# Kernel optimization log

Measured on AMD Instinct MI355X. Metric: run time of the kernel, lower is better.

## Reference

```python
import jax, jax.numpy as jnp
import numpy as np

B, S, D = 2, 2048, 2048
H, KV, HD = 8, 1, 256          # num_heads, num_kv_heads, head_dim
ROPE_BASE = 10000.0
NEG_INF = -1e9


def _rope_cos_sin(position_ids, head_dim, base):
    # position_ids: [B, S] -> cos/sin: [B, S, head_dim]
    inv_freq = 1.0 / (base ** (jnp.arange(0, head_dim, 2, dtype=jnp.float32) / head_dim))
    freqs = position_ids.astype(jnp.float32)[..., None] * inv_freq  # [B,S,HD/2]
    emb = jnp.concatenate([freqs, freqs], axis=-1)                  # [B,S,HD]
    return jnp.cos(emb), jnp.sin(emb)


def _rotate_half(x):
    h = x.shape[-1] // 2
    return jnp.concatenate([-x[..., h:], x[..., :h]], axis=-1)


def _apply_rope(x, cos, sin):
    # x: [B,h,S,HD]; cos/sin: [B,S,HD]
    c = cos[:, None, :, :]
    s = sin[:, None, :, :]
    return x * c + _rotate_half(x) * s


def setup_inputs() -> dict:
    key = jax.random.key(0)
    ks = jax.random.split(key, 6)
    hidden_state = jax.random.normal(ks[0], (B, S, D), dtype=jnp.float32)
    # additive causal mask: 0 on/below diagonal, -inf above
    causal = jnp.tril(jnp.ones((S, S), dtype=bool))
    attention_mask = jnp.where(causal, 0.0, NEG_INF).astype(jnp.float32)[None, None]  # [B?1,1,S,S]
    attention_mask = jnp.broadcast_to(attention_mask, (B, 1, S, S))
    position_ids = jnp.broadcast_to(jnp.arange(S, dtype=jnp.int64)[None, :], (B, S))
    scale = 0.02
    Wq = jax.random.normal(ks[1], (D, H * HD), dtype=jnp.float32) * scale
    Wk = jax.random.normal(ks[2], (D, KV * HD), dtype=jnp.float32) * scale
    Wv = jax.random.normal(ks[3], (D, KV * HD), dtype=jnp.float32) * scale
    Wo = jax.random.normal(ks[4], (H * HD, D), dtype=jnp.float32) * scale
    return {"hidden_state": hidden_state, "attention_mask": attention_mask,
            "position_ids": position_ids, "Wq": Wq, "Wk": Wk, "Wv": Wv, "Wo": Wo}


def reference(hidden_state, attention_mask, position_ids, Wq, Wk, Wv, Wo):
    bsz, q_len, _ = hidden_state.shape
    n_rep = H // KV
    # projections
    q = (hidden_state @ Wq).reshape(bsz, q_len, H, HD).transpose(0, 2, 1, 3)   # [B,H,S,HD]
    k = (hidden_state @ Wk).reshape(bsz, q_len, KV, HD).transpose(0, 2, 1, 3)  # [B,KV,S,HD]
    v = (hidden_state @ Wv).reshape(bsz, q_len, KV, HD).transpose(0, 2, 1, 3)
    # RoPE
    cos, sin = _rope_cos_sin(position_ids, HD, ROPE_BASE)
    q = _apply_rope(q, cos, sin)
    k = _apply_rope(k, cos, sin)
    # GQA: repeat kv heads
    k = jnp.repeat(k, n_rep, axis=1)  # [B,H,S,HD]
    v = jnp.repeat(v, n_rep, axis=1)
    # eager attention with full score matrix (faithful to source)
    scores = jnp.einsum('bhqd,bhkd->bhqk', q, k) / jnp.sqrt(jnp.float32(HD))
    scores = scores + attention_mask
    attn = jax.nn.softmax(scores.astype(jnp.float32), axis=-1).astype(q.dtype)
    out = jnp.einsum('bhqk,bhkd->bhqd', attn, v)            # [B,H,S,HD]
    out = out.transpose(0, 2, 1, 3).reshape(bsz, q_len, H * HD)
    return out @ Wo
```

## Files before the change

kernel.cpp:

```cpp
#include <hip/hip_runtime.h>
#include <cstdint>
#include <cstddef>

#define B_   2
#define S_   2048
#define D_   2048
#define H_   8
#define HD_  256
#define M_   (B_ * S_)
#define NQ_  (H_ * HD_)
#define NKV_ 256

typedef unsigned short u16;
typedef __attribute__((ext_vector_type(8))) short short8v;
typedef __attribute__((ext_vector_type(4))) float f32x4;

__device__ __forceinline__ u16 f2bf_rn(float x) {
    unsigned int u = __float_as_uint(x);
    unsigned int r = u + 0x7FFFu + ((u >> 16) & 1u);
    return (u16)(r >> 16);
}
__device__ __forceinline__ float bf2f(u16 h) {
    return __uint_as_float(((unsigned int)h) << 16);
}

__global__ __launch_bounds__(256) void split_kernel(const float* __restrict__ in,
                                                    u16* __restrict__ hi,
                                                    u16* __restrict__ lo)
{
    const size_t i = ((size_t)blockIdx.x * 256 + threadIdx.x) * 8;
    float4 v0 = *(const float4*)(in + i);
    float4 v1 = *(const float4*)(in + i + 4);
    float xs[8] = {v0.x, v0.y, v0.z, v0.w, v1.x, v1.y, v1.z, v1.w};
    unsigned int hv[4], lv[4];
#pragma unroll
    for (int k = 0; k < 4; ++k) {
        u16 h0 = f2bf_rn(xs[2 * k]);
        u16 h1 = f2bf_rn(xs[2 * k + 1]);
        u16 l0 = f2bf_rn(xs[2 * k] - bf2f(h0));
        u16 l1 = f2bf_rn(xs[2 * k + 1] - bf2f(h1));
        hv[k] = (unsigned int)h0 | ((unsigned int)h1 << 16);
        lv[k] = (unsigned int)l0 | ((unsigned int)l1 << 16);
    }
    *(uint4*)(hi + i) = make_uint4(hv[0], hv[1], hv[2], hv[3]);
    *(uint4*)(lo + i) = make_uint4(lv[0], lv[1], lv[2], lv[3]);
}

__global__ __launch_bounds__(256) void tsplit_kernel(const float* __restrict__ W,
                                                     u16* __restrict__ Th,
                                                     u16* __restrict__ Tl,
                                                     int K, int N)
{
    __shared__ float t[64][65];
    const int kt = blockIdx.x, nt = blockIdx.y;
    const int c4 = (threadIdx.x & 15) * 4;
    const int r  = threadIdx.x >> 4;

#pragma unroll
    for (int s = 0; s < 4; ++s) {
        const int kk = r + s * 16;
        float4 v = *(const float4*)(W + (size_t)(kt * 64 + kk) * N + nt * 64 + c4);
        t[kk][c4 + 0] = v.x;
        t[kk][c4 + 1] = v.y;
        t[kk][c4 + 2] = v.z;
        t[kk][c4 + 3] = v.w;
    }
    __syncthreads();
#pragma unroll
    for (int s = 0; s < 4; ++s) {
        const int nn = r + s * 16;
        unsigned int hv[2], lv[2];
#pragma unroll
        for (int p = 0; p < 2; ++p) {
            u16 h0, h1, l0, l1;
            float x0 = t[c4 + 2 * p][nn];
            float x1 = t[c4 + 2 * p + 1][nn];
            h0 = f2bf_rn(x0); l0 = f2bf_rn(x0 - bf2f(h0));
            h1 = f2bf_rn(x1); l1 = f2bf_rn(x1 - bf2f(h1));
            hv[p] = (unsigned int)h0 | ((unsigned int)h1 << 16);
            lv[p] = (unsigned int)l0 | ((unsigned int)l1 << 16);
        }
        u16* ph = Th + (size_t)(nt * 64 + nn) * K + kt * 64 + c4;
        u16* pl = Tl + (size_t)(nt * 64 + nn) * K + kt * 64 + c4;
        *(uint2*)ph = make_uint2(hv[0], hv[1]);
        *(uint2*)pl = make_uint2(lv[0], lv[1]);
    }
}

__device__ __forceinline__ void mfma_gemm_tile(
    const u16* __restrict__ Ah, const u16* __restrict__ Al,
    const u16* __restrict__ Bh, const u16* __restrict__ Bl,
    float* __restrict__ C, const int Kd, const int ldc,
    const int bm0, const int bn0)
{
    __shared__ u16 ldsAh[128 * 32];
    __shared__ u16 ldsAl[128 * 32];
    __shared__ u16 ldsBh[128 * 32];
    __shared__ u16 ldsBl[128 * 32];

    const int tid  = threadIdx.x;
    const int lane = tid & 63;
    const int w    = tid >> 6;
    const int wr   = w >> 1, wc = w & 1;

    const int rs = tid >> 2;
    const int qs = (tid & 3) * 8;

    const u16* pAh = Ah + (size_t)(bm0 + rs) * Kd + qs;
    const u16* pAl = Al + (size_t)(bm0 + rs) * Kd + qs;
    const u16* pBh = Bh + (size_t)(bn0 + rs) * Kd + qs;
    const u16* pBl = Bl + (size_t)(bn0 + rs) * Kd + qs;
    const size_t rowskip = (size_t)64 * Kd;

    f32x4 acc[4][4];
#pragma unroll
    for (int i = 0; i < 4; ++i)
#pragma unroll
        for (int j = 0; j < 4; ++j) acc[i][j] = (f32x4){0.f, 0.f, 0.f, 0.f};

    const int fr = lane & 15;
    const int kb = (lane >> 4) * 8;

    for (int k0 = 0; k0 < Kd; k0 += 32) {
        uint4 sAh0 = *(const uint4*)(pAh);
        uint4 sAh1 = *(const uint4*)(pAh + rowskip);
        uint4 sAl0 = *(const uint4*)(pAl);
        uint4 sAl1 = *(const uint4*)(pAl + rowskip);
        uint4 sBh0 = *(const uint4*)(pBh);
        uint4 sBh1 = *(const uint4*)(pBh + rowskip);
        uint4 sBl0 = *(const uint4*)(pBl);
        uint4 sBl1 = *(const uint4*)(pBl + rowskip);
        pAh += 32; pAl += 32; pBh += 32; pBl += 32;

        if (k0) __syncthreads();
        *(uint4*)&ldsAh[rs * 32 + qs]        = sAh0;
        *(uint4*)&ldsAh[(rs + 64) * 32 + qs] = sAh1;
        *(uint4*)&ldsAl[rs * 32 + qs]        = sAl0;
        *(uint4*)&ldsAl[(rs + 64) * 32 + qs] = sAl1;
        *(uint4*)&ldsBh[rs * 32 + qs]        = sBh0;
        *(uint4*)&ldsBh[(rs + 64) * 32 + qs] = sBh1;
        *(uint4*)&ldsBl[rs * 32 + qs]        = sBl0;
        *(uint4*)&ldsBl[(rs + 64) * 32 + qs] = sBl1;
        __syncthreads();

        short8v a_h[4], a_l[4], b_h[4], b_l[4];
#pragma unroll
        for (int f = 0; f < 4; ++f) {
            const int ra = (wr * 64 + f * 16 + fr) * 32 + kb;
            const int rb = (wc * 64 + f * 16 + fr) * 32 + kb;
            a_h[f] = *(const short8v*)&ldsAh[ra];
            a_l[f] = *(const short8v*)&ldsAl[ra];
            b_h[f] = *(const short8v*)&ldsBh[rb];
            b_l[f] = *(const short8v*)&ldsBl[rb];
        }
#pragma unroll
        for (int i = 0; i < 4; ++i)
#pragma unroll
            for (int j = 0; j < 4; ++j) {
                acc[i][j] = __builtin_amdgcn_mfma_f32_16x16x32_bf16(a_h[i], b_h[j], acc[i][j], 0, 0, 0);
                acc[i][j] = __builtin_amdgcn_mfma_f32_16x16x32_bf16(a_h[i], b_l[j], acc[i][j], 0, 0, 0);
                acc[i][j] = __builtin_amdgcn_mfma_f32_16x16x32_bf16(a_l[i], b_h[j], acc[i][j], 0, 0, 0);
            }
    }

    const int cr = (lane >> 4) * 4;
    const int cc = lane & 15;
#pragma unroll
    for (int i = 0; i < 4; ++i)
#pragma unroll
        for (int j = 0; j < 4; ++j) {
#pragma unroll
            for (int r = 0; r < 4; ++r) {
                C[(size_t)(bm0 + wr * 64 + i * 16 + cr + r) * ldc
                  + (bn0 + wc * 64 + j * 16 + cc)] = acc[i][j][r];
            }
        }
}

__global__ __launch_bounds__(256, 2) void qkv_mfma_kernel(
    const u16* __restrict__ Xh, const u16* __restrict__ Xl,
    const u16* __restrict__ WqTh, const u16* __restrict__ WqTl,
    const u16* __restrict__ WkTh, const u16* __restrict__ WkTl,
    const u16* __restrict__ WvTh, const u16* __restrict__ WvTl,
    float* __restrict__ Qo, float* __restrict__ Ko, float* __restrict__ Vo)
{
    const int bn = blockIdx.x;
    const u16 *Bh, *Bl; float* C; int ldc, col0;
    if (bn < 16)      { Bh = WqTh; Bl = WqTl; C = Qo; ldc = NQ_;  col0 = bn * 128; }
    else if (bn < 18) { Bh = WkTh; Bl = WkTl; C = Ko; ldc = NKV_; col0 = (bn - 16) * 128; }
    else              { Bh = WvTh; Bl = WvTl; C = Vo; ldc = NKV_; col0 = (bn - 18) * 128; }
    mfma_gemm_tile(Xh, Xl, Bh, Bl, C, D_, ldc, blockIdx.y * 128, col0);
}

__global__ __launch_bounds__(256, 2) void out_mfma_kernel(
    const u16* __restrict__ Ch, const u16* __restrict__ Cl,
    const u16* __restrict__ WoTh, const u16* __restrict__ WoTl,
    float* __restrict__ Out)
{
    mfma_gemm_tile(Ch, Cl, WoTh, WoTl, Out, NQ_, D_, blockIdx.y * 128, blockIdx.x * 128);
}

__global__ __launch_bounds__(128) void rope_split_q_kernel(
    const float* __restrict__ Qw, u16* __restrict__ Qh, u16* __restrict__ Ql)
{
    const int row = blockIdx.x;
    const int d = threadIdx.x;
    const int s = row & (S_ - 1);

    const float expo = (float)(2 * d) / (float)HD_;
    const float inv_freq = 1.0f / powf(10000.0f, expo);
    float sn, c;
    sincosf((float)s * inv_freq, &sn, &c);

    const float* qr = Qw + (size_t)row * NQ_;
    u16* qhr = Qh + (size_t)row * NQ_;
    u16* qlr = Ql + (size_t)row * NQ_;
#pragma unroll
    for (int h = 0; h < H_; ++h) {
        float x0 = qr[h * HD_ + d];
        float x1 = qr[h * HD_ + d + 128];
        float y0 = x0 * c - x1 * sn;
        float y1 = x1 * c + x0 * sn;
        u16 h0 = f2bf_rn(y0), h1 = f2bf_rn(y1);
        qhr[h * HD_ + d]       = h0;
        qhr[h * HD_ + d + 128] = h1;
        qlr[h * HD_ + d]       = f2bf_rn(y0 - bf2f(h0));
        qlr[h * HD_ + d + 128] = f2bf_rn(y1 - bf2f(h1));
    }
}

__global__ __launch_bounds__(128) void rope_split_k_kernel(
    const float* __restrict__ Kw, u16* __restrict__ Kh, u16* __restrict__ Kl)
{
    const int row = blockIdx.x;
    const int d = threadIdx.x;
    const int s = row & (S_ - 1);

    const float expo = (float)(2 * d) / (float)HD_;
    const float inv_freq = 1.0f / powf(10000.0f, expo);
    float sn, c;
    sincosf((float)s * inv_freq, &sn, &c);

    const float* kr = Kw + (size_t)row * HD_;
    float x0 = kr[d], x1 = kr[d + 128];
    float y0 = x0 * c - x1 * sn;
    float y1 = x1 * c + x0 * sn;
    u16 h0 = f2bf_rn(y0), h1 = f2bf_rn(y1);
    Kh[(size_t)row * HD_ + d]       = h0;
    Kh[(size_t)row * HD_ + d + 128] = h1;
    Kl[(size_t)row * HD_ + d]       = f2bf_rn(y0 - bf2f(h0));
    Kl[(size_t)row * HD_ + d + 128] = f2bf_rn(y1 - bf2f(h1));
}

#define KVB_ 32

__global__ __launch_bounds__(256, 2) void attn_mfma_kernel(
    const u16* __restrict__ Qh, const u16* __restrict__ Ql,
    const u16* __restrict__ Kh, const u16* __restrict__ Kl,
    const u16* __restrict__ VtH, const u16* __restrict__ VtL,
    float* __restrict__ O)
{
    __shared__ u16 kv[2 * 256 * 40];
    __shared__ u16 pb[2 * 64 * 40];

    const int tid = threadIdx.x;
    const int lane = tid & 63;
    const int w = tid >> 6;

    const int u = blockIdx.x & 255;
    const int pair = blockIdx.x >> 8;
    const int qt_base = u & 31;
    const int qt = pair ? (31 - qt_base) : qt_base;
    const int bh = (u >> 5) + pair * 8;
    const int b = bh >> 3, h = bh & 7;

    const int fr = lane & 15;
    const int kq = (lane >> 4);
    const int xm = fr & 7;

    short8v qfh[8], qfl[8];
    {
        const size_t qrow = (size_t)(b * S_ + qt * 64 + w * 16 + fr);
        const u16* ph = Qh + qrow * NQ_ + h * HD_ + kq * 8;
        const u16* pl = Ql + qrow * NQ_ + h * HD_ + kq * 8;
#pragma unroll
        for (int ks = 0; ks < 8; ++ks) {
            qfh[ks] = *(const short8v*)(ph + ks * 32);
            qfl[ks] = *(const short8v*)(pl + ks * 32);
        }
    }

    f32x4 oacc[16];
#pragma unroll
    for (int f = 0; f < 16; ++f) oacc[f] = (f32x4){0.f, 0.f, 0.f, 0.f};
    float m_i[4] = {-1e30f, -1e30f, -1e30f, -1e30f};
    float l_i[4] = {0.f, 0.f, 0.f, 0.f};

    const u16* ksrc[2] = {Kh + (size_t)b * S_ * HD_, Kl + (size_t)b * S_ * HD_};
    const u16* vsrc[2] = {VtH + (size_t)b * HD_ * S_, VtL + (size_t)b * HD_ * S_};

    const int nkt = (qt + 1) * 2;

#pragma unroll
    for (int c = 0; c < 2; ++c) {
        const u16* s = ksrc[c];
#pragma unroll
        for (int i = 0; i < 4; ++i) {
            const int chunk = i * 256 + tid;
            const int row = chunk >> 5, ch = chunk & 31;
            uint4 v = *(const uint4*)(s + (size_t)row * HD_ + ch * 8);
            *(uint4*)&kv[c * 8192 + row * 256 + (ch ^ (row & 7)) * 8] = v;
        }
    }
    __syncthreads();

    for (int kt = 0; kt < nkt; ++kt) {
        f32x4 s0 = (f32x4){0.f, 0.f, 0.f, 0.f};
        f32x4 s1 = (f32x4){0.f, 0.f, 0.f, 0.f};
#pragma unroll
        for (int ks = 0; ks < 8; ++ks) {
            const int ch = (ks * 4 + kq) ^ xm;
            short8v kh0 = *(const short8v*)&kv[fr * 256 + ch * 8];
            short8v kh1 = *(const short8v*)&kv[(16 + fr) * 256 + ch * 8];
            short8v kl0 = *(const short8v*)&kv[8192 + fr * 256 + ch * 8];
            short8v kl1 = *(const short8v*)&kv[8192 + (16 + fr) * 256 + ch * 8];
            s0 = __builtin_amdgcn_mfma_f32_16x16x32_bf16(qfh[ks], kh0, s0, 0, 0, 0);
            s1 = __builtin_amdgcn_mfma_f32_16x16x32_bf16(qfh[ks], kh1, s1, 0, 0, 0);
            s0 = __builtin_amdgcn_mfma_f32_16x16x32_bf16(qfh[ks], kl0, s0, 0, 0, 0);
            s1 = __builtin_amdgcn_mfma_f32_16x16x32_bf16(qfh[ks], kl1, s1, 0, 0, 0);
            s0 = __builtin_amdgcn_mfma_f32_16x16x32_bf16(qfl[ks], kh0, s0, 0, 0, 0);
            s1 = __builtin_amdgcn_mfma_f32_16x16x32_bf16(qfl[ks], kh1, s1, 0, 0, 0);
        }

        const int qglob = qt * 64 + w * 16 + kq * 4;
        const int kg = kt * KVB_ + fr;
#pragma unroll
        for (int r = 0; r < 4; ++r) {
            float x0 = s0[r] * 0.0625f;
            float x1 = s1[r] * 0.0625f;
            if (kg > qglob + r)      x0 = -1e30f;
            if (kg + 16 > qglob + r) x1 = -1e30f;
            float mx = fmaxf(x0, x1);
#pragma unroll
            for (int off = 1; off < 16; off <<= 1)
                mx = fmaxf(mx, __shfl_xor(mx, off, 64));
            const float mnew = fmaxf(m_i[r], mx);
            const float alpha = __expf(m_i[r] - mnew);
            const float p0 = __expf(x0 - mnew);
            const float p1 = __expf(x1 - mnew);
            float ps = p0 + p1;
#pragma unroll
            for (int off = 1; off < 16; off <<= 1)
                ps += __shfl_xor(ps, off, 64);
            l_i[r] = l_i[r] * alpha + ps;
            m_i[r] = mnew;
#pragma unroll
            for (int f = 0; f < 16; ++f) oacc[f][r] *= alpha;

            const int prow = (w * 16 + kq * 4 + r) * 40;
            u16 h0 = f2bf_rn(p0), h1 = f2bf_rn(p1);
            pb[prow + fr]             = h0;
            pb[prow + 16 + fr]        = h1;
            pb[2560 + prow + fr]      = f2bf_rn(p0 - bf2f(h0));
            pb[2560 + prow + 16 + fr] = f2bf_rn(p1 - bf2f(h1));
        }
        __syncthreads();

#pragma unroll
        for (int c = 0; c < 2; ++c) {
            const u16* s = vsrc[c] + (size_t)kt * KVB_;
#pragma unroll
            for (int i = 0; i < 4; ++i) {
                const int chunk = i * 256 + tid;
                const int d = chunk >> 2, ch = chunk & 3;
                uint4 v = *(const uint4*)(s + (size_t)d * S_ + ch * 8);
                *(uint4*)&kv[c * 10240 + d * 40 + ch * 8] = v;
            }
        }
        __syncthreads();

        {
            short8v pah = *(const short8v*)&pb[(w * 16 + fr) * 40 + kq * 8];
            short8v pal = *(const short8v*)&pb[2560 + (w * 16 + fr) * 40 + kq * 8];
#pragma unroll
            for (int f = 0; f < 16; ++f) {
                const int vrow = (f * 16 + fr) * 40 + kq * 8;
                short8v vh = *(const short8v*)&kv[vrow];
                short8v vl = *(const short8v*)&kv[10240 + vrow];
                oacc[f] = __builtin_amdgcn_mfma_f32_16x16x32_bf16(pah, vh, oacc[f], 0, 0, 0);
                oacc[f] = __builtin_amdgcn_mfma_f32_16x16x32_bf16(pal, vh, oacc[f], 0, 0, 0);
                oacc[f] = __builtin_amdgcn_mfma_f32_16x16x32_bf16(pah, vl, oacc[f], 0, 0, 0);
            }
        }
        __syncthreads();

        if (kt + 1 < nkt) {
#pragma unroll
            for (int c = 0; c < 2; ++c) {
                const u16* s = ksrc[c] + (size_t)(kt + 1) * KVB_ * HD_;
#pragma unroll
                for (int i = 0; i < 4; ++i) {
                    const int chunk = i * 256 + tid;
                    const int row = chunk >> 5, ch = chunk & 31;
                    uint4 v = *(const uint4*)(s + (size_t)row * HD_ + ch * 8);
                    *(uint4*)&kv[c * 8192 + row * 256 + (ch ^ (row & 7)) * 8] = v;
                }
            }
            __syncthreads();
        }
    }

    float* orow = O + (size_t)(b * S_ + qt * 64 + w * 16 + kq * 4) * NQ_ + h * HD_ + fr;
#pragma unroll
    for (int r = 0; r < 4; ++r) {
        const float inv_l = 1.0f / l_i[r];
#pragma unroll
        for (int f = 0; f < 16; ++f)
            orow[(size_t)r * NQ_ + f * 16] = oacc[f][r] * inv_l;
    }
}

extern "C" void kernel_launch(void* const* d_in, const int* in_sizes, int n_in,
                              void* d_out, int out_size, void* d_ws, size_t ws_size,
                              hipStream_t stream)
{
    (void)in_sizes; (void)n_in; (void)out_size; (void)ws_size;

    const float* hidden = (const float*)d_in[0];
    const float* Wq = (const float*)d_in[3];
    const float* Wk = (const float*)d_in[4];
    const float* Wv = (const float*)d_in[5];
    const float* Wo = (const float*)d_in[6];
    float* out = (float*)d_out;

    char* ws = (char*)d_ws;
    float* Qw = (float*)(ws + 0);
    u16* Kh2 = (u16*)(ws + 0);
    u16* Kl2 = (u16*)(ws + 2097152u);
    u16* VtH = (u16*)(ws + 4194304u);
    u16* VtL = (u16*)(ws + 6291456u);
    float* Kw = (float*)(ws + 33554432u);
    float* Vw = (float*)(ws + 37748736u);
    float* Cw = (float*)(ws + 41943040u);
    u16* Ah  = (u16*)(ws + 75497472u);
    u16* Al  = (u16*)(ws + 92274688u);
    u16* WqTh = (u16*)(ws + 109051904u);
    u16* WqTl = (u16*)(ws + 117440512u);
    u16* WkTh = (u16*)(ws + 125829120u);
    u16* WkTl = (u16*)(ws + 126877696u);
    u16* WvTh = (u16*)(ws + 127926272u);
    u16* WvTl = (u16*)(ws + 128974848u);
    u16* WoTh = WqTh;
    u16* WoTl = WqTl;
    u16* Qhb = Ah;
    u16* Qlb = Al;

    split_kernel<<<dim3((M_ * D_) / (256 * 8)), dim3(256), 0, stream>>>(hidden, Ah, Al);

    tsplit_kernel<<<dim3(D_ / 64, NQ_ / 64),  dim3(256), 0, stream>>>(Wq, WqTh, WqTl, D_, NQ_);
    tsplit_kernel<<<dim3(D_ / 64, NKV_ / 64), dim3(256), 0, stream>>>(Wk, WkTh, WkTl, D_, NKV_);
    tsplit_kernel<<<dim3(D_ / 64, NKV_ / 64), dim3(256), 0, stream>>>(Wv, WvTh, WvTl, D_, NKV_);

    qkv_mfma_kernel<<<dim3(20, M_ / 128), dim3(256), 0, stream>>>(
        Ah, Al, WqTh, WqTl, WkTh, WkTl, WvTh, WvTl, Qw, Kw, Vw);

    rope_split_q_kernel<<<dim3(M_), dim3(128), 0, stream>>>(Qw, Qhb, Qlb);

    rope_split_k_kernel<<<dim3(M_), dim3(128), 0, stream>>>(Kw, Kh2, Kl2);

    tsplit_kernel<<<dim3(S_ / 64, NKV_ / 64), dim3(256), 0, stream>>>(
        Vw, VtH, VtL, S_, NKV_);
    tsplit_kernel<<<dim3(S_ / 64, NKV_ / 64), dim3(256), 0, stream>>>(
        Vw + (size_t)S_ * NKV_, VtH + (size_t)HD_ * S_, VtL + (size_t)HD_ * S_, S_, NKV_);

    attn_mfma_kernel<<<dim3(512), dim3(256), 0, stream>>>(
        Qhb, Qlb, Kh2, Kl2, VtH, VtL, Cw);

    split_kernel<<<dim3((M_ * NQ_) / (256 * 8)), dim3(256), 0, stream>>>(Cw, Ah, Al);

    tsplit_kernel<<<dim3(NQ_ / 64, D_ / 64), dim3(256), 0, stream>>>(Wo, WoTh, WoTl, NQ_, D_);

    out_mfma_kernel<<<dim3(D_ / 128, M_ / 128), dim3(256), 0, stream>>>(
        Ah, Al, WoTh, WoTl, out);
}
```

Measured before the change: 678.9 us.

## Prefetch K/V tiles into registers in attention and use direct global-to-LDS loads in GEMM

The attention kernel now issues global loads for the next K tile and the next V tile into registers before the current tile's compute, then writes them to LDS afterward. This hides global-memory latency behind the MFMA work. The P buffer row stride is padded from 40 to 44 to cut LDS bank conflicts. Query-tile ordering changes so blocks run longest-first, and the GEMM tile loader switches to global_load_lds builtins that bypass VGPR staging. The register prefetch raises register pressure in a kernel bound to 2 blocks per CU.

```diff
diff --git a/kernel.cpp b/kernel.cpp
--- a/kernel.cpp
+++ b/kernel.cpp
@@ -24,6 +24,12 @@
     return __uint_as_float(((unsigned int)h) << 16);
 }
 
+__device__ __forceinline__ void gll16(const u16* g, u16* l) {
+    __builtin_amdgcn_global_load_lds(
+        (const __attribute__((address_space(1))) void*)(g),
+        (__attribute__((address_space(3))) void*)(l), 16, 0, 0);
+}
+
 __global__ __launch_bounds__(256) void split_kernel(const float* __restrict__ in,
                                                     u16* __restrict__ hi,
                                                     u16* __restrict__ lo)
@@ -103,14 +109,12 @@
     const int w    = tid >> 6;
     const int wr   = w >> 1, wc = w & 1;
 
-    const int rs = tid >> 2;
-    const int qs = (tid & 3) * 8;
-
-    const u16* pAh = Ah + (size_t)(bm0 + rs) * Kd + qs;
-    const u16* pAl = Al + (size_t)(bm0 + rs) * Kd + qs;
-    const u16* pBh = Bh + (size_t)(bn0 + rs) * Kd + qs;
-    const u16* pBl = Bl + (size_t)(bn0 + rs) * Kd + qs;
-    const size_t rowskip = (size_t)64 * Kd;
+    const int srow = w * 32 + (lane >> 2);
+    const int schk = (lane & 3) * 8;
+    const u16* gAh = Ah + (size_t)(bm0 + srow) * Kd + schk;
+    const u16* gAl = Al + (size_t)(bm0 + srow) * Kd + schk;
+    const u16* gBh = Bh + (size_t)(bn0 + srow) * Kd + schk;
+    const u16* gBl = Bl + (size_t)(bn0 + srow) * Kd + schk;
 
     f32x4 acc[4][4];
 #pragma unroll
@@ -122,25 +126,16 @@
     const int kb = (lane >> 4) * 8;
 
     for (int k0 = 0; k0 < Kd; k0 += 32) {
-        uint4 sAh0 = *(const uint4*)(pAh);
-        uint4 sAh1 = *(const uint4*)(pAh + rowskip);
-        uint4 sAl0 = *(const uint4*)(pAl);
-        uint4 sAl1 = *(const uint4*)(pAl + rowskip);
-        uint4 sBh0 = *(const uint4*)(pBh);
-        uint4 sBh1 = *(const uint4*)(pBh + rowskip);
-        uint4 sBl0 = *(const uint4*)(pBl);
-        uint4 sBl1 = *(const uint4*)(pBl + rowskip);
-        pAh += 32; pAl += 32; pBh += 32; pBl += 32;
-
         if (k0) __syncthreads();
-        *(uint4*)&ldsAh[rs * 32 + qs]        = sAh0;
-        *(uint4*)&ldsAh[(rs + 64) * 32 + qs] = sAh1;
-        *(uint4*)&ldsAl[rs * 32 + qs]        = sAl0;
-        *(uint4*)&ldsAl[(rs + 64) * 32 + qs] = sAl1;
-        *(uint4*)&ldsBh[rs * 32 + qs]        = sBh0;
-        *(uint4*)&ldsBh[(rs + 64) * 32 + qs] = sBh1;
-        *(uint4*)&ldsBl[rs * 32 + qs]        = sBl0;
-        *(uint4*)&ldsBl[(rs + 64) * 32 + qs] = sBl1;
+#pragma unroll
+        for (int c = 0; c < 2; ++c) {
+            const size_t go = (size_t)(c * 16) * Kd + k0;
+            const int lb = (w * 32 + c * 16) * 32;
+            gll16(gAh + go, &ldsAh[lb]);
+            gll16(gAl + go, &ldsAl[lb]);
+            gll16(gBh + go, &ldsBh[lb]);
+            gll16(gBl + go, &ldsBl[lb]);
+        }
         __syncthreads();
 
         short8v a_h[4], a_l[4], b_h[4], b_l[4];
@@ -253,6 +248,7 @@
 }
 
 #define KVB_ 32
+#define PBS_ 44
 
 __global__ __launch_bounds__(256, 2) void attn_mfma_kernel(
     const u16* __restrict__ Qh, const u16* __restrict__ Ql,
@@ -261,7 +257,7 @@
     float* __restrict__ O)
 {
     __shared__ u16 kv[2 * 256 * 40];
-    __shared__ u16 pb[2 * 64 * 40];
+    __shared__ u16 pb[2 * 64 * PBS_];
 
     const int tid = threadIdx.x;
     const int lane = tid & 63;
@@ -269,8 +265,7 @@
 
     const int u = blockIdx.x & 255;
     const int pair = blockIdx.x >> 8;
-    const int qt_base = u & 31;
-    const int qt = pair ? (31 - qt_base) : qt_base;
+    const int qt = 31 - (u & 31);
     const int bh = (u >> 5) + pair * 8;
     const int b = bh >> 3, h = bh & 7;
 
@@ -301,6 +296,8 @@
 
     const int nkt = (qt + 1) * 2;
 
+    uint4 kreg[2][4], vreg[2][4];
+
 #pragma unroll
     for (int c = 0; c < 2; ++c) {
         const u16* s = ksrc[c];
@@ -312,9 +309,33 @@
             *(uint4*)&kv[c * 8192 + row * 256 + (ch ^ (row & 7)) * 8] = v;
         }
     }
+#pragma unroll
+    for (int c = 0; c < 2; ++c) {
+#pragma unroll
+        for (int i = 0; i < 4; ++i) {
+            const int chunk = i * 256 + tid;
+            const int d = chunk >> 2, ch = chunk & 3;
+            vreg[c][i] = *(const uint4*)(vsrc[c] + (size_t)d * S_ + ch * 8);
+        }
+    }
     __syncthreads();
 
     for (int kt = 0; kt < nkt; ++kt) {
+        const bool more = (kt + 1 < nkt);
+
+        if (more) {
+#pragma unroll
+            for (int c = 0; c < 2; ++c) {
+                const u16* s = ksrc[c] + (size_t)(kt + 1) * KVB_ * HD_;
+#pragma unroll
+                for (int i = 0; i < 4; ++i) {
+                    const int chunk = i * 256 + tid;
+                    const int row = chunk >> 5, ch = chunk & 31;
+                    kreg[c][i] = *(const uint4*)(s + (size_t)row * HD_ + ch * 8);
+                }
+            }
+        }
+
         f32x4 s0 = (f32x4){0.f, 0.f, 0.f, 0.f};
         f32x4 s1 = (f32x4){0.f, 0.f, 0.f, 0.f};
 #pragma unroll
@@ -357,31 +378,41 @@
 #pragma unroll
             for (int f = 0; f < 16; ++f) oacc[f][r] *= alpha;
 
-            const int prow = (w * 16 + kq * 4 + r) * 40;
+            const int prow = (w * 16 + kq * 4 + r) * PBS_;
             u16 h0 = f2bf_rn(p0), h1 = f2bf_rn(p1);
-            pb[prow + fr]             = h0;
-            pb[prow + 16 + fr]        = h1;
-            pb[2560 + prow + fr]      = f2bf_rn(p0 - bf2f(h0));
-            pb[2560 + prow + 16 + fr] = f2bf_rn(p1 - bf2f(h1));
+            pb[prow + fr]                    = h0;
+            pb[prow + 16 + fr]               = h1;
+            pb[64 * PBS_ + prow + fr]        = f2bf_rn(p0 - bf2f(h0));
+            pb[64 * PBS_ + prow + 16 + fr]   = f2bf_rn(p1 - bf2f(h1));
         }
         __syncthreads();
 
 #pragma unroll
-        for (int c = 0; c < 2; ++c) {
-            const u16* s = vsrc[c] + (size_t)kt * KVB_;
+        for (int c = 0; c < 2; ++c)
 #pragma unroll
             for (int i = 0; i < 4; ++i) {
                 const int chunk = i * 256 + tid;
                 const int d = chunk >> 2, ch = chunk & 3;
-                uint4 v = *(const uint4*)(s + (size_t)d * S_ + ch * 8);
-                *(uint4*)&kv[c * 10240 + d * 40 + ch * 8] = v;
+                *(uint4*)&kv[c * 10240 + d * 40 + ch * 8] = vreg[c][i];
             }
-        }
         __syncthreads();
 
+        if (more) {
+#pragma unroll
+            for (int c = 0; c < 2; ++c) {
+                const u16* s = vsrc[c] + (size_t)(kt + 1) * KVB_;
+#pragma unroll
+                for (int i = 0; i < 4; ++i) {
+                    const int chunk = i * 256 + tid;
+                    const int d = chunk >> 2, ch = chunk & 3;
+                    vreg[c][i] = *(const uint4*)(s + (size_t)d * S_ + ch * 8);
+                }
+            }
+        }
+
         {
-            short8v pah = *(const short8v*)&pb[(w * 16 + fr) * 40 + kq * 8];
-            short8v pal = *(const short8v*)&pb[2560 + (w * 16 + fr) * 40 + kq * 8];
+            short8v pah = *(const short8v*)&pb[(w * 16 + fr) * PBS_ + kq * 8];
+            short8v pal = *(const short8v*)&pb[64 * PBS_ + (w * 16 + fr) * PBS_ + kq * 8];
 #pragma unroll
             for (int f = 0; f < 16; ++f) {
                 const int vrow = (f * 16 + fr) * 40 + kq * 8;
@@ -392,20 +423,17 @@
                 oacc[f] = __builtin_amdgcn_mfma_f32_16x16x32_bf16(pah, vl, oacc[f], 0, 0, 0);
             }
         }
-        __syncthreads();
-
-        if (kt + 1 < nkt) {
-#pragma unroll
-            for (int c = 0; c < 2; ++c) {
-                const u16* s = ksrc[c] + (size_t)(kt + 1) * KVB_ * HD_;
+
+        if (more) {
+            __syncthreads();
+#pragma unroll
+            for (int c = 0; c < 2; ++c)
 #pragma unroll
                 for (int i = 0; i < 4; ++i) {
                     const int chunk = i * 256 + tid;
                     const int row = chunk >> 5, ch = chunk & 31;
-                    uint4 v = *(const uint4*)(s + (size_t)row * HD_ + ch * 8);
-                    *(uint4*)&kv[c * 8192 + row * 256 + (ch ^ (row & 7)) * 8] = v;
+                    *(uint4*)&kv[c * 8192 + row * 256 + (ch ^ (row & 7)) * 8] = kreg[c][i];
                 }
-            }
             __syncthreads();
         }
     }
@@ -465,7 +493,6 @@
         Ah, Al, WqTh, WqTl, WkTh, WkTl, WvTh, WvTl, Qw, Kw, Vw);
 
     rope_split_q_kernel<<<dim3(M_), dim3(128), 0, stream>>>(Qw, Qhb, Qlb);
-
     rope_split_k_kernel<<<dim3(M_), dim3(128), 0, stream>>>(Kw, Kh2, Kl2);
 
     tsplit_kernel<<<dim3(S_ / 64, NKV_ / 64), dim3(256), 0, stream>>>(
```

Result: slower. 1.018 ms (+50.0%).
